# Optimization experiments

Measured on AMD Instinct MI355X. Metric: run time of the kernel, lower is better.

## Reference

```python
import jax, jax.numpy as jnp
from jax import lax
import numpy as np

B, S = 128, 512
TARGET_SIZE = 32
T = TARGET_SIZE + 4  # tag_size, START = T-2, END = T-1


def setup_inputs() -> dict:
    key = jax.random.key(0)
    k1, k2, k3, k4 = jax.random.split(key, 4)
    feats = jax.random.normal(k1, (B, S, T), dtype=jnp.float32)
    # contiguous-prefix mask (lengths in [S//2, S])
    lengths = jax.random.randint(k2, (B,), S // 2, S + 1)
    mask = (jnp.arange(S)[None, :] < lengths[:, None]).astype(jnp.int32)
    tags = jax.random.randint(k3, (B, S), 0, TARGET_SIZE).astype(jnp.int32)
    # learned transitions, with the hard constraints from __init__
    transitions = 0.1 * jax.random.normal(k4, (T, T), dtype=jnp.float32)
    transitions = transitions.at[:, T - 2].set(-1000.0)  # nothing -> START
    transitions = transitions.at[T - 1, :].set(-1000.0)  # END -> nothing
    return {"feats": feats, "transitions": transitions, "mask": mask, "tags": tags}


def _nll(feats, transitions, mask, tags):
    # feats: (B,S,T), transitions: (T,T) with [i,j] = score(prev=i -> cur=j)
    b, s, t = feats.shape
    START, END = t - 2, t - 1
    fdtype = feats.dtype

    feats_t = jnp.swapaxes(feats, 0, 1)   # (S,B,T)
    mask_t = jnp.swapaxes(mask, 0, 1)     # (S,B)

    # ---- forward algorithm (partition function) ----
    # scores[t,b,i,j] = feats[b,t,j] + transitions[i,j]
    part0 = feats_t[0] + transitions[START][None, :]  # (B,T): alpha after step 0

    def step(part, xs):
        f_step, m_step = xs  # (B,T), (B,)
        # cur[b,i,j] = feats[b,j] + trans[i,j] + part[b,i]
        cur = f_step[:, None, :] + transitions[None, :, :] + part[:, :, None]
        new_part = jax.nn.logsumexp(cur, axis=1)  # (B,T)
        part = jnp.where(m_step[:, None].astype(bool), new_part, part)
        return part, None

    part, _ = lax.scan(step, part0, (feats_t[1:], mask_t[1:]))
    final = jax.nn.logsumexp(part[:, :, None] + transitions[None, :, :], axis=1)  # (B,T)
    forward_score = jnp.sum(final[:, END])

    # ---- gold score ----
    tags_i = tags.astype(jnp.int32)
    prev_tags = jnp.concatenate(
        [jnp.full((b, 1), START, dtype=jnp.int32), tags_i[:, :-1]], axis=1)  # (B,S)
    emit = jnp.take_along_axis(feats, tags_i[:, :, None], axis=2)[:, :, 0]    # (B,S)
    trans_sc = transitions[prev_tags, tags_i]                                  # (B,S)
    tg_energy = jnp.sum((emit + trans_sc) * mask.astype(fdtype))
    lengths = jnp.sum(mask, axis=1).astype(jnp.int32)                          # (B,)
    end_ids = jnp.take_along_axis(tags_i, (lengths - 1)[:, None], axis=1)[:, 0]
    end_energy = jnp.sum(transitions[end_ids, END])
    gold_score = tg_energy + end_energy

    # average_batch = True
    return (forward_score - gold_score) / jnp.asarray(b, fdtype)


def reference(feats, transitions, mask, tags):
    return _nll(feats, transitions, mask, tags)
```

## Files before the change

### kernel.cpp

```cpp
#include <hip/hip_runtime.h>


namespace {
constexpr int kB = 128;
constexpr int kS = 512;
constexpr int kT = 36;
constexpr int kStart = 34;
constexpr int kEnd = 35;

__device__ __forceinline__ float readlane_f(float v, int lane) {
    return __builtin_bit_cast(float, __builtin_amdgcn_readlane(__builtin_bit_cast(int, v), lane));
}

__device__ __forceinline__ float wave_sum(float v) {
#pragma unroll
    for (int off = 32; off; off >>= 1) v += __shfl_xor(v, off, 64);
    return v;
}

__device__ __forceinline__ int wave_sum_i(int v) {
#pragma unroll
    for (int off = 32; off; off >>= 1) v += __shfl_xor(v, off, 64);
    return v;
}

#define FOR36(X) \
    X(0, 0) X(1, 1) X(2, 2) X(3, 3) X(4, 0) X(5, 1) X(6, 2) X(7, 3) \
    X(8, 0) X(9, 1) X(10, 2) X(11, 3) X(12, 0) X(13, 1) X(14, 2) X(15, 3) \
    X(16, 0) X(17, 1) X(18, 2) X(19, 3) X(20, 0) X(21, 1) X(22, 2) X(23, 3) \
    X(24, 0) X(25, 1) X(26, 2) X(27, 3) X(28, 0) X(29, 1) X(30, 2) X(31, 3) \
    X(32, 0) X(33, 1) X(34, 2) X(35, 3)

#define FMDECL(n, a) float Fm##n;
#define FMINIT(n, a) Fm##n = __expf(trans[(n)*kT + jc]);
#define BMDECL(n, a) float Bm##n;
#define BMINIT(n, a) Bm##n = __expf(trans[jc * kT + (n)]);
#define FDOT(n, a) v##a = fmaf(readlane_f(q, n), Fm##n, v##a);
#define BDOT(n, a) w##a = fmaf(readlane_f(p, n), Bm##n, w##a);

#define LDF(t) fl[(size_t)(((t) < kS - 1) ? (t) : (kS - 1)) * kT]
#define LDBW(t) fl[(size_t)(((t) > 0) ? (t) : 0) * kT]

__global__ __attribute__((amdgpu_flat_work_group_size(128, 128),
                          amdgpu_waves_per_eu(1, 1)))
void crf_split_kernel(const float* __restrict__ feats,
                      const float* __restrict__ trans,
                      const int* __restrict__ mask,
                      const int* __restrict__ tags,
                      float* __restrict__ out) {
    const int b = blockIdx.x;
    const int tid = threadIdx.x;
    const int w = tid >> 6;
    const int j = tid & 63;
    const int jc = (j < kT) ? j : (kT - 1);
    const float* fbase = feats + (size_t)b * kS * kT;
    const float* fl = fbase + jc;
    const int* mb = mask + b * kS;
    const int* tb = tags + b * kS;

    __shared__ float gbuf[64];
    __shared__ float cbbuf;

    int len = 0;
#pragma unroll
    for (int k = 0; k < kS / 64; ++k) len += mb[k * 64 + j];
    len = wave_sum_i(len);

    float q = 0.f, Cf = 0.f;

    if (w == 1) {
        FOR36(BMDECL)
        FOR36(BMINIT)
        float g = (j < kT) ? __expf(trans[j * kT + kEnd]) : 0.f;
        float Cb = 0.f;

        auto bstep = [&](float eb, int tau) {
            const float p = eb * g;
            float w0 = 0.f, w1 = 0.f, w2 = 0.f, w3 = 0.f;
            FOR36(BDOT)
            const float ng = (w0 + w1) + (w2 + w3);
            g = (tau < len) ? ng : g;
        };
        auto renormB = [&]() {
            const float mg = readlane_f(g, 0);
            g *= __builtin_amdgcn_rcpf(mg);
            Cb += __logf(mg);
        };

        float pA0, pA1, pA2, pA3, pA4, pA5, pA6, pA7;
        float pB0, pB1, pB2, pB3, pB4, pB5, pB6, pB7;
        float eA0, eA1, eA2, eA3, eA4, eA5, eA6, eA7;
        pA0 = LDBW(511); pA1 = LDBW(510); pA2 = LDBW(509); pA3 = LDBW(508);
        pA4 = LDBW(507); pA5 = LDBW(506); pA6 = LDBW(505); pA7 = LDBW(504);
        eA0 = __expf(pA0); eA1 = __expf(pA1); eA2 = __expf(pA2); eA3 = __expf(pA3);
        eA4 = __expf(pA4); eA5 = __expf(pA5); eA6 = __expf(pA6); eA7 = __expf(pA7);

        int it0 = 0;
        while (it0 < kS / 2) {
            pB0 = LDBW(503 - it0); pB1 = LDBW(502 - it0); pB2 = LDBW(501 - it0); pB3 = LDBW(500 - it0);
            pB4 = LDBW(499 - it0); pB5 = LDBW(498 - it0); pB6 = LDBW(497 - it0); pB7 = LDBW(496 - it0);
            bstep(eA0, 511 - it0); bstep(eA1, 510 - it0);
            bstep(eA2, 509 - it0); bstep(eA3, 508 - it0);
            renormB();
            bstep(eA4, 507 - it0); bstep(eA5, 506 - it0);
            bstep(eA6, 505 - it0); bstep(eA7, 504 - it0);
            renormB();
            eA0 = __expf(pB0); eA1 = __expf(pB1); eA2 = __expf(pB2); eA3 = __expf(pB3);
            eA4 = __expf(pB4); eA5 = __expf(pB5); eA6 = __expf(pB6); eA7 = __expf(pB7);

            pA0 = LDBW(495 - it0); pA1 = LDBW(494 - it0); pA2 = LDBW(493 - it0); pA3 = LDBW(492 - it0);
            pA4 = LDBW(491 - it0); pA5 = LDBW(490 - it0); pA6 = LDBW(489 - it0); pA7 = LDBW(488 - it0);
            bstep(eA0, 503 - it0); bstep(eA1, 502 - it0);
            bstep(eA2, 501 - it0); bstep(eA3, 500 - it0);
            renormB();
            bstep(eA4, 499 - it0); bstep(eA5, 498 - it0);
            bstep(eA6, 497 - it0); bstep(eA7, 496 - it0);
            renormB();
            eA0 = __expf(pA0); eA1 = __expf(pA1); eA2 = __expf(pA2); eA3 = __expf(pA3);
            eA4 = __expf(pA4); eA5 = __expf(pA5); eA6 = __expf(pA6); eA7 = __expf(pA7);
            it0 += 16;
        }
        gbuf[j] = g;
        if (j == 0) cbbuf = Cb;
    } else {
        FOR36(FMDECL)
        FOR36(FMINIT)
        const float a0 = (j < kT) ? (fl[0] + trans[kStart * kT + jc]) : -1e30f;
        Cf = readlane_f(a0, 0);
        q = __expf(a0 - Cf);

        auto fstep = [&](float ef, int t) {
            float v0 = 0.f, v1 = 0.f, v2 = 0.f, v3 = 0.f;
            FOR36(FDOT)
            const float nq = ((v0 + v1) + (v2 + v3)) * ef;
            q = (t < kS / 2) ? nq : q;
        };
        auto renormF = [&]() {
            const float mf = readlane_f(q, 0);
            q *= __builtin_amdgcn_rcpf(mf);
            Cf += __logf(mf);
        };

        float pA0, pA1, pA2, pA3, pA4, pA5, pA6, pA7;
        float pB0, pB1, pB2, pB3, pB4, pB5, pB6, pB7;
        float eA0, eA1, eA2, eA3, eA4, eA5, eA6, eA7;
        pA0 = LDF(1); pA1 = LDF(2); pA2 = LDF(3); pA3 = LDF(4);
        pA4 = LDF(5); pA5 = LDF(6); pA6 = LDF(7); pA7 = LDF(8);
        eA0 = __expf(pA0); eA1 = __expf(pA1); eA2 = __expf(pA2); eA3 = __expf(pA3);
        eA4 = __expf(pA4); eA5 = __expf(pA5); eA6 = __expf(pA6); eA7 = __expf(pA7);

        int it0 = 0;
        while (it0 < kS / 2) {
            pB0 = LDF(it0 + 9);  pB1 = LDF(it0 + 10); pB2 = LDF(it0 + 11); pB3 = LDF(it0 + 12);
            pB4 = LDF(it0 + 13); pB5 = LDF(it0 + 14); pB6 = LDF(it0 + 15); pB7 = LDF(it0 + 16);
            fstep(eA0, it0 + 1); fstep(eA1, it0 + 2);
            fstep(eA2, it0 + 3); fstep(eA3, it0 + 4);
            renormF();
            fstep(eA4, it0 + 5); fstep(eA5, it0 + 6);
            fstep(eA6, it0 + 7); fstep(eA7, it0 + 8);
            renormF();
            eA0 = __expf(pB0); eA1 = __expf(pB1); eA2 = __expf(pB2); eA3 = __expf(pB3);
            eA4 = __expf(pB4); eA5 = __expf(pB5); eA6 = __expf(pB6); eA7 = __expf(pB7);

            pA0 = LDF(it0 + 17); pA1 = LDF(it0 + 18); pA2 = LDF(it0 + 19); pA3 = LDF(it0 + 20);
            pA4 = LDF(it0 + 21); pA5 = LDF(it0 + 22); pA6 = LDF(it0 + 23); pA7 = LDF(it0 + 24);
            fstep(eA0, it0 + 9);  fstep(eA1, it0 + 10);
            fstep(eA2, it0 + 11); fstep(eA3, it0 + 12);
            renormF();
            fstep(eA4, it0 + 13); fstep(eA5, it0 + 14);
            fstep(eA6, it0 + 15); fstep(eA7, it0 + 16);
            renormF();
            eA0 = __expf(pA0); eA1 = __expf(pA1); eA2 = __expf(pA2); eA3 = __expf(pA3);
            eA4 = __expf(pA4); eA5 = __expf(pA5); eA6 = __expf(pA6); eA7 = __expf(pA7);
            it0 += 16;
        }
    }

    __syncthreads();

    if (w == 0) {
        const float Z = wave_sum(q * gbuf[j]);
        const float forward_b = Cf + cbbuf + __logf(Z);

        float gold = 0.f;
        for (int k = j; k < kS; k += 64) {
            if (k < len) {
                const int tg = tb[k];
                const int pv = (k == 0) ? kStart : tb[k - 1];
                gold += fbase[(size_t)k * kT + tg] + trans[pv * kT + tg];
            }
        }
        gold = wave_sum(gold);

        if (j == 0) {
            gold += trans[tb[len - 1] * kT + kEnd];
            atomicAdd(out, (forward_b - gold) * (1.0f / kB));
        }
    }
}

}

extern "C" void kernel_launch(void* const* d_in, const int* in_sizes, int n_in,
                              void* d_out, int out_size, void* d_ws, size_t ws_size,
                              hipStream_t stream) {
    const float* feats = (const float*)d_in[0];
    const float* trans = (const float*)d_in[1];
    const int* mask = (const int*)d_in[2];
    const int* tags = (const int*)d_in[3];
    float* out = (float*)d_out;

    (void)hipMemsetAsync(out, 0, sizeof(float), stream);
    crf_split_kernel<<<dim3(kB), dim3(128), 0, stream>>>(feats, trans, mask, tags, out);
}
```

Measured before the change: 102.9 us.

## Trim CRF matvec to 34 source tags and fold renormalization into emissions

Drops the START and END source rows from the per-step dot product, since transitions into START are -1000 and END has no outgoing transitions, so their exp terms are negligible. Moves each renormalization off the recurrence's critical path by scaling the next step's emission factor by the reciprocal instead of rescaling the state. All 34 readlanes are now issued before the FMAs behind a scheduling barrier. The forward loop gets an exact-length tail, which removes the per-step t<S/2 select. This cuts per-step latency on the serial chain, but the 34-row truncation is approximate and relies on the -1000 transition constraints.

```diff
diff --git a/kernel.cpp b/kernel.cpp
--- a/kernel.cpp
+++ b/kernel.cpp
@@ -24,19 +24,20 @@
     return v;
 }
 
-#define FOR36(X) \
+#define FOR34(X) \
     X(0, 0) X(1, 1) X(2, 2) X(3, 3) X(4, 0) X(5, 1) X(6, 2) X(7, 3) \
     X(8, 0) X(9, 1) X(10, 2) X(11, 3) X(12, 0) X(13, 1) X(14, 2) X(15, 3) \
     X(16, 0) X(17, 1) X(18, 2) X(19, 3) X(20, 0) X(21, 1) X(22, 2) X(23, 3) \
     X(24, 0) X(25, 1) X(26, 2) X(27, 3) X(28, 0) X(29, 1) X(30, 2) X(31, 3) \
-    X(32, 0) X(33, 1) X(34, 2) X(35, 3)
+    X(32, 0) X(33, 1)
 
 #define FMDECL(n, a) float Fm##n;
 #define FMINIT(n, a) Fm##n = __expf(trans[(n)*kT + jc]);
 #define BMDECL(n, a) float Bm##n;
 #define BMINIT(n, a) Bm##n = __expf(trans[jc * kT + (n)]);
-#define FDOT(n, a) v##a = fmaf(readlane_f(q, n), Fm##n, v##a);
-#define BDOT(n, a) w##a = fmaf(readlane_f(p, n), Bm##n, w##a);
+#define RLD(n, a) const float s##n = readlane_f(src, n);
+#define FD(n, a) v##a = fmaf(s##n, Fm##n, v##a);
+#define BD(n, a) w##a = fmaf(s##n, Bm##n, w##a);
 
 #define LDF(t) fl[(size_t)(((t) < kS - 1) ? (t) : (kS - 1)) * kT]
 #define LDBW(t) fl[(size_t)(((t) > 0) ? (t) : 0) * kT]
@@ -69,22 +70,25 @@
     float q = 0.f, Cf = 0.f;
 
     if (w == 1) {
-        FOR36(BMDECL)
-        FOR36(BMINIT)
+        FOR34(BMDECL)
+        FOR34(BMINIT)
         float g = (j < kT) ? __expf(trans[j * kT + kEnd]) : 0.f;
         float Cb = 0.f;
 
         auto bstep = [&](float eb, int tau) {
-            const float p = eb * g;
+            const float src = eb * g;
             float w0 = 0.f, w1 = 0.f, w2 = 0.f, w3 = 0.f;
-            FOR36(BDOT)
+            FOR34(RLD)
+            __builtin_amdgcn_sched_barrier(0);
+            FOR34(BD)
             const float ng = (w0 + w1) + (w2 + w3);
             g = (tau < len) ? ng : g;
         };
-        auto renormB = [&]() {
+        auto renormB = [&](float& eb_next, int tau_next) {
             const float mg = readlane_f(g, 0);
-            g *= __builtin_amdgcn_rcpf(mg);
-            Cb += __logf(mg);
+            const float lg = __logf(mg);
+            const float r = __builtin_amdgcn_rcpf(mg);
+            if (tau_next < len) { Cb += lg; eb_next *= r; }
         };
 
         float pA0, pA1, pA2, pA3, pA4, pA5, pA6, pA7;
@@ -101,44 +105,46 @@
             pB4 = LDBW(499 - it0); pB5 = LDBW(498 - it0); pB6 = LDBW(497 - it0); pB7 = LDBW(496 - it0);
             bstep(eA0, 511 - it0); bstep(eA1, 510 - it0);
             bstep(eA2, 509 - it0); bstep(eA3, 508 - it0);
-            renormB();
+            renormB(eA4, 507 - it0);
             bstep(eA4, 507 - it0); bstep(eA5, 506 - it0);
             bstep(eA6, 505 - it0); bstep(eA7, 504 - it0);
-            renormB();
             eA0 = __expf(pB0); eA1 = __expf(pB1); eA2 = __expf(pB2); eA3 = __expf(pB3);
             eA4 = __expf(pB4); eA5 = __expf(pB5); eA6 = __expf(pB6); eA7 = __expf(pB7);
+            renormB(eA0, 503 - it0);
 
             pA0 = LDBW(495 - it0); pA1 = LDBW(494 - it0); pA2 = LDBW(493 - it0); pA3 = LDBW(492 - it0);
             pA4 = LDBW(491 - it0); pA5 = LDBW(490 - it0); pA6 = LDBW(489 - it0); pA7 = LDBW(488 - it0);
             bstep(eA0, 503 - it0); bstep(eA1, 502 - it0);
             bstep(eA2, 501 - it0); bstep(eA3, 500 - it0);
-            renormB();
+            renormB(eA4, 499 - it0);
             bstep(eA4, 499 - it0); bstep(eA5, 498 - it0);
             bstep(eA6, 497 - it0); bstep(eA7, 496 - it0);
-            renormB();
             eA0 = __expf(pA0); eA1 = __expf(pA1); eA2 = __expf(pA2); eA3 = __expf(pA3);
             eA4 = __expf(pA4); eA5 = __expf(pA5); eA6 = __expf(pA6); eA7 = __expf(pA7);
+            if (it0 < kS / 2 - 16) renormB(eA0, 495 - it0);
             it0 += 16;
         }
         gbuf[j] = g;
         if (j == 0) cbbuf = Cb;
     } else {
-        FOR36(FMDECL)
-        FOR36(FMINIT)
+        FOR34(FMDECL)
+        FOR34(FMINIT)
         const float a0 = (j < kT) ? (fl[0] + trans[kStart * kT + jc]) : -1e30f;
         Cf = readlane_f(a0, 0);
         q = __expf(a0 - Cf);
 
-        auto fstep = [&](float ef, int t) {
+        auto fstep = [&](float ef) {
+            const float src = q;
             float v0 = 0.f, v1 = 0.f, v2 = 0.f, v3 = 0.f;
-            FOR36(FDOT)
-            const float nq = ((v0 + v1) + (v2 + v3)) * ef;
-            q = (t < kS / 2) ? nq : q;
-        };
-        auto renormF = [&]() {
+            FOR34(RLD)
+            __builtin_amdgcn_sched_barrier(0);
+            FOR34(FD)
+            q = ((v0 + v1) + (v2 + v3)) * ef;
+        };
+        auto renormF = [&](float& ef_next) {
             const float mf = readlane_f(q, 0);
-            q *= __builtin_amdgcn_rcpf(mf);
             Cf += __logf(mf);
+            ef_next *= __builtin_amdgcn_rcpf(mf);
         };
 
         float pA0, pA1, pA2, pA3, pA4, pA5, pA6, pA7;
@@ -150,30 +156,37 @@
         eA4 = __expf(pA4); eA5 = __expf(pA5); eA6 = __expf(pA6); eA7 = __expf(pA7);
 
         int it0 = 0;
-        while (it0 < kS / 2) {
+        while (it0 < 240) {
             pB0 = LDF(it0 + 9);  pB1 = LDF(it0 + 10); pB2 = LDF(it0 + 11); pB3 = LDF(it0 + 12);
             pB4 = LDF(it0 + 13); pB5 = LDF(it0 + 14); pB6 = LDF(it0 + 15); pB7 = LDF(it0 + 16);
-            fstep(eA0, it0 + 1); fstep(eA1, it0 + 2);
-            fstep(eA2, it0 + 3); fstep(eA3, it0 + 4);
-            renormF();
-            fstep(eA4, it0 + 5); fstep(eA5, it0 + 6);
-            fstep(eA6, it0 + 7); fstep(eA7, it0 + 8);
-            renormF();
+            fstep(eA0); fstep(eA1); fstep(eA2); fstep(eA3);
+            renormF(eA4);
+            fstep(eA4); fstep(eA5); fstep(eA6); fstep(eA7);
             eA0 = __expf(pB0); eA1 = __expf(pB1); eA2 = __expf(pB2); eA3 = __expf(pB3);
             eA4 = __expf(pB4); eA5 = __expf(pB5); eA6 = __expf(pB6); eA7 = __expf(pB7);
+            renormF(eA0);
 
             pA0 = LDF(it0 + 17); pA1 = LDF(it0 + 18); pA2 = LDF(it0 + 19); pA3 = LDF(it0 + 20);
             pA4 = LDF(it0 + 21); pA5 = LDF(it0 + 22); pA6 = LDF(it0 + 23); pA7 = LDF(it0 + 24);
-            fstep(eA0, it0 + 9);  fstep(eA1, it0 + 10);
-            fstep(eA2, it0 + 11); fstep(eA3, it0 + 12);
-            renormF();
-            fstep(eA4, it0 + 13); fstep(eA5, it0 + 14);
-            fstep(eA6, it0 + 15); fstep(eA7, it0 + 16);
-            renormF();
+            fstep(eA0); fstep(eA1); fstep(eA2); fstep(eA3);
+            renormF(eA4);
+            fstep(eA4); fstep(eA5); fstep(eA6); fstep(eA7);
             eA0 = __expf(pA0); eA1 = __expf(pA1); eA2 = __expf(pA2); eA3 = __expf(pA3);
             eA4 = __expf(pA4); eA5 = __expf(pA5); eA6 = __expf(pA6); eA7 = __expf(pA7);
+            renormF(eA0);
             it0 += 16;
         }
+        float pT0 = LDF(249), pT1 = LDF(250), pT2 = LDF(251), pT3 = LDF(252);
+        float pT4 = LDF(253), pT5 = LDF(254), pT6 = LDF(255);
+        fstep(eA0); fstep(eA1); fstep(eA2); fstep(eA3);
+        renormF(eA4);
+        fstep(eA4); fstep(eA5); fstep(eA6); fstep(eA7);
+        float eT0 = __expf(pT0), eT1 = __expf(pT1), eT2 = __expf(pT2), eT3 = __expf(pT3);
+        float eT4 = __expf(pT4), eT5 = __expf(pT5), eT6 = __expf(pT6);
+        renormF(eT0);
+        fstep(eT0); fstep(eT1); fstep(eT2); fstep(eT3);
+        renormF(eT4);
+        fstep(eT4); fstep(eT5); fstep(eT6);
     }
 
     __syncthreads();
```

Result: slower. 106.0 us (+3.0%).

## Replace readlane matvec with DPP ring-rotation matvec across lane groups

Applied to the files above, without the earlier changes.

The per-step 36x36 matrix-vector product is reorganized. Before, it used 36 scalar readlanes per step. Now each lane holds three state components and does a systolic-style ring rotation with DPP row_ror over 16-lane rows, followed by shuffles to gather the result. The aim is to remove the serialized readlane/SALU path and spread the work over lane groups with fewer dependent operations per step. In exchange it adds DPP rotation latency, three ds_bpermute shuffles per step, renormalization once every four steps instead of every four in an eight-step pattern, and more delicate indexing math.

```diff
diff --git a/kernel.cpp b/kernel.cpp
--- a/kernel.cpp
+++ b/kernel.cpp
@@ -11,175 +11,169 @@
 __device__ __forceinline__ float readlane_f(float v, int lane) {
     return __builtin_bit_cast(float, __builtin_amdgcn_readlane(__builtin_bit_cast(int, v), lane));
 }
+__device__ __forceinline__ float ror1_f(float x) {
+    const int xi = __builtin_bit_cast(int, x);
+    return __builtin_bit_cast(float, __builtin_amdgcn_update_dpp(xi, xi, 0x121, 0xF, 0xF, false));
+}
+__device__ __forceinline__ float ror8_f(float x) {
+    const int xi = __builtin_bit_cast(int, x);
+    return __builtin_bit_cast(float, __builtin_amdgcn_update_dpp(xi, xi, 0x128, 0xF, 0xF, false));
+}
 
 __device__ __forceinline__ float wave_sum(float v) {
 #pragma unroll
     for (int off = 32; off; off >>= 1) v += __shfl_xor(v, off, 64);
     return v;
 }
-
 __device__ __forceinline__ int wave_sum_i(int v) {
 #pragma unroll
     for (int off = 32; off; off >>= 1) v += __shfl_xor(v, off, 64);
     return v;
 }
 
-#define FOR36(X) \
-    X(0, 0) X(1, 1) X(2, 2) X(3, 3) X(4, 0) X(5, 1) X(6, 2) X(7, 3) \
-    X(8, 0) X(9, 1) X(10, 2) X(11, 3) X(12, 0) X(13, 1) X(14, 2) X(15, 3) \
-    X(16, 0) X(17, 1) X(18, 2) X(19, 3) X(20, 0) X(21, 1) X(22, 2) X(23, 3) \
-    X(24, 0) X(25, 1) X(26, 2) X(27, 3) X(28, 0) X(29, 1) X(30, 2) X(31, 3) \
-    X(32, 0) X(33, 1) X(34, 2) X(35, 3)
-
-#define FMDECL(n, a) float Fm##n;
-#define FMINIT(n, a) Fm##n = __expf(trans[(n)*kT + jc]);
-#define BMDECL(n, a) float Bm##n;
-#define BMINIT(n, a) Bm##n = __expf(trans[jc * kT + (n)]);
-#define FDOT(n, a) v##a = fmaf(readlane_f(q, n), Fm##n, v##a);
-#define BDOT(n, a) w##a = fmaf(readlane_f(p, n), Bm##n, w##a);
-
-#define LDF(t) fl[(size_t)(((t) < kS - 1) ? (t) : (kS - 1)) * kT]
-#define LDBW(t) fl[(size_t)(((t) > 0) ? (t) : 0) * kT]
+#define FOR8(X) X(0) X(1) X(2) X(3) X(4) X(5) X(6) X(7)
+
+#define XPC(row, col) ((((row) < kT) && ((col) < kT)) ? __expf(trans[(row)*kT + (col)]) : 0.f)
+#define JO(m) (16 * rc + ((p - (m)) & 15))
+
+#define FDU(k) const float DU0_##k = XPC(s0, JO(k)), DU1_##k = XPC(s1, JO(k)), DU2_##k = XPC(s2, JO(k));
+#define FDV(k) const float DV0_##k = XPC(s0, JO(8 + (k))), DV1_##k = XPC(s1, JO(8 + (k))), DV2_##k = XPC(s2, JO(8 + (k)));
+#define BDU(k) const float DU0_##k = XPC(JO(k), s0), DU1_##k = XPC(JO(k), s1), DU2_##k = XPC(JO(k), s2);
+#define BDV(k) const float DV0_##k = XPC(JO(8 + (k)), s0), DV1_##k = XPC(JO(8 + (k)), s1), DV2_##k = XPC(JO(8 + (k)), s2);
+
+#define PHASE(k) \
+    U = fmaf(R0, DU0_##k, U); V = fmaf(R0, DV0_##k, V); \
+    U = fmaf(R1, DU1_##k, U); V = fmaf(R1, DV1_##k, V); \
+    U = fmaf(R2, DU2_##k, U); V = fmaf(R2, DV2_##k, V); \
+    U = ror1_f(U); V = ror1_f(V);
+
+#define LD3(t, s) p##s##x = fl0[(t) * kT]; p##s##y = fl1[(t) * kT]; p##s##z = fl2[(t) * kT];
+#define EX3(s) e##s##x = __expf(p##s##x); e##s##y = __expf(p##s##y); e##s##z = __expf(p##s##z);
 
 __global__ __attribute__((amdgpu_flat_work_group_size(128, 128),
                           amdgpu_waves_per_eu(1, 1)))
-void crf_split_kernel(const float* __restrict__ feats,
-                      const float* __restrict__ trans,
-                      const int* __restrict__ mask,
-                      const int* __restrict__ tags,
-                      float* __restrict__ out) {
+void crf_ring_kernel(const float* __restrict__ feats,
+                     const float* __restrict__ trans,
+                     const int* __restrict__ mask,
+                     const int* __restrict__ tags,
+                     float* __restrict__ out) {
     const int b = blockIdx.x;
     const int tid = threadIdx.x;
     const int w = tid >> 6;
     const int j = tid & 63;
-    const int jc = (j < kT) ? j : (kT - 1);
+    const int p = j & 15;
+    const int rr = j >> 4;
+    const int rc = (rr < 2) ? rr : 2;
+    const int s0 = p, s1 = 16 + p, s2 = 32 + p;
     const float* fbase = feats + (size_t)b * kS * kT;
-    const float* fl = fbase + jc;
+    const float* fl0 = fbase + s0;
+    const float* fl1 = fbase + s1;
+    const float* fl2 = fbase + ((s2 < kT) ? s2 : (kT - 1));
     const int* mb = mask + b * kS;
     const int* tb = tags + b * kS;
 
-    __shared__ float gbuf[64];
+    __shared__ float gbuf[3][64];
     __shared__ float cbbuf;
 
     int len = 0;
 #pragma unroll
     for (int k = 0; k < kS / 64; ++k) len += mb[k * 64 + j];
-    len = wave_sum_i(len);
-
-    float q = 0.f, Cf = 0.f;
+    len = __builtin_amdgcn_readfirstlane(wave_sum_i(len));
+
+    float Q0 = 0.f, Q1 = 0.f, Q2 = 0.f, Cf = 0.f;
+
+    float p0x, p0y, p0z, p1x, p1y, p1z, p2x, p2y, p2z, p3x, p3y, p3z;
+    float e0x, e0y, e0z, e1x, e1y, e1z, e2x, e2y, e2z, e3x, e3y, e3z;
 
     if (w == 1) {
-        FOR36(BMDECL)
-        FOR36(BMINIT)
-        float g = (j < kT) ? __expf(trans[j * kT + kEnd]) : 0.f;
+        FOR8(BDU) FOR8(BDV)
+        float G0 = __expf(trans[s0 * kT + kEnd]);
+        float G1 = __expf(trans[s1 * kT + kEnd]);
+        float G2 = (s2 < kT) ? __expf(trans[s2 * kT + kEnd]) : 0.f;
         float Cb = 0.f;
 
-        auto bstep = [&](float eb, int tau) {
-            const float p = eb * g;
-            float w0 = 0.f, w1 = 0.f, w2 = 0.f, w3 = 0.f;
-            FOR36(BDOT)
-            const float ng = (w0 + w1) + (w2 + w3);
-            g = (tau < len) ? ng : g;
-        };
-        auto renormB = [&]() {
-            const float mg = readlane_f(g, 0);
-            g *= __builtin_amdgcn_rcpf(mg);
-            Cb += __logf(mg);
-        };
-
-        float pA0, pA1, pA2, pA3, pA4, pA5, pA6, pA7;
-        float pB0, pB1, pB2, pB3, pB4, pB5, pB6, pB7;
-        float eA0, eA1, eA2, eA3, eA4, eA5, eA6, eA7;
-        pA0 = LDBW(511); pA1 = LDBW(510); pA2 = LDBW(509); pA3 = LDBW(508);
-        pA4 = LDBW(507); pA5 = LDBW(506); pA6 = LDBW(505); pA7 = LDBW(504);
-        eA0 = __expf(pA0); eA1 = __expf(pA1); eA2 = __expf(pA2); eA3 = __expf(pA3);
-        eA4 = __expf(pA4); eA5 = __expf(pA5); eA6 = __expf(pA6); eA7 = __expf(pA7);
-
-        int it0 = 0;
-        while (it0 < kS / 2) {
-            pB0 = LDBW(503 - it0); pB1 = LDBW(502 - it0); pB2 = LDBW(501 - it0); pB3 = LDBW(500 - it0);
-            pB4 = LDBW(499 - it0); pB5 = LDBW(498 - it0); pB6 = LDBW(497 - it0); pB7 = LDBW(496 - it0);
-            bstep(eA0, 511 - it0); bstep(eA1, 510 - it0);
-            bstep(eA2, 509 - it0); bstep(eA3, 508 - it0);
-            renormB();
-            bstep(eA4, 507 - it0); bstep(eA5, 506 - it0);
-            bstep(eA6, 505 - it0); bstep(eA7, 504 - it0);
-            renormB();
-            eA0 = __expf(pB0); eA1 = __expf(pB1); eA2 = __expf(pB2); eA3 = __expf(pB3);
-            eA4 = __expf(pB4); eA5 = __expf(pB5); eA6 = __expf(pB6); eA7 = __expf(pB7);
-
-            pA0 = LDBW(495 - it0); pA1 = LDBW(494 - it0); pA2 = LDBW(493 - it0); pA3 = LDBW(492 - it0);
-            pA4 = LDBW(491 - it0); pA5 = LDBW(490 - it0); pA6 = LDBW(489 - it0); pA7 = LDBW(488 - it0);
-            bstep(eA0, 503 - it0); bstep(eA1, 502 - it0);
-            bstep(eA2, 501 - it0); bstep(eA3, 500 - it0);
-            renormB();
-            bstep(eA4, 499 - it0); bstep(eA5, 498 - it0);
-            bstep(eA6, 497 - it0); bstep(eA7, 496 - it0);
-            renormB();
-            eA0 = __expf(pA0); eA1 = __expf(pA1); eA2 = __expf(pA2); eA3 = __expf(pA3);
-            eA4 = __expf(pA4); eA5 = __expf(pA5); eA6 = __expf(pA6); eA7 = __expf(pA7);
-            it0 += 16;
-        }
-        gbuf[j] = g;
+        auto bstep = [&](float e0, float e1, float e2, int tau) {
+            const float R0 = e0 * G0, R1 = e1 * G1, R2 = e2 * G2;
+            float U = 0.f, V = 0.f;
+            FOR8(PHASE)
+            const float Y = ror8_f(U) + V;
+            const float n0 = __shfl(Y, s0, 64);
+            const float n1 = __shfl(Y, s1, 64);
+            const float n2 = __shfl(Y, s2, 64);
+            const bool upd = tau < len;
+            G0 = upd ? n0 : G0; G1 = upd ? n1 : G1; G2 = upd ? n2 : G2;
+        };
+        auto renormB = [&](float& e0, float& e1, float& e2, int tau_next) {
+            const float mg = readlane_f(G0, 0);
+            const float lg = __logf(mg);
+            const float rv = __builtin_amdgcn_rcpf(mg);
+            if (tau_next < len) { Cb += lg; e0 *= rv; e1 *= rv; e2 *= rv; }
+        };
+
+        LD3(511, 0) LD3(510, 1) LD3(509, 2) LD3(508, 3)
+        EX3(0) EX3(1) EX3(2) EX3(3)
+        LD3(507, 0) LD3(506, 1) LD3(505, 2) LD3(504, 3)
+
+#pragma unroll 1
+        for (int g = 0; g < 64; ++g) {
+            const int tg = 511 - 4 * g;
+            bstep(e0x, e0y, e0z, tg);
+            bstep(e1x, e1y, e1z, tg - 1);
+            bstep(e2x, e2y, e2z, tg - 2);
+            bstep(e3x, e3y, e3z, tg - 3);
+            EX3(0) EX3(1) EX3(2) EX3(3)
+            LD3(tg - 8, 0) LD3(tg - 9, 1) LD3(tg - 10, 2) LD3(tg - 11, 3)
+            if (g < 63) renormB(e0x, e0y, e0z, tg - 4);
+        }
+        gbuf[0][j] = G0; gbuf[1][j] = G1; gbuf[2][j] = G2;
         if (j == 0) cbbuf = Cb;
     } else {
-        FOR36(FMDECL)
-        FOR36(FMINIT)
-        const float a0 = (j < kT) ? (fl[0] + trans[kStart * kT + jc]) : -1e30f;
-        Cf = readlane_f(a0, 0);
-        q = __expf(a0 - Cf);
-
-        auto fstep = [&](float ef, int t) {
-            float v0 = 0.f, v1 = 0.f, v2 = 0.f, v3 = 0.f;
-            FOR36(FDOT)
-            const float nq = ((v0 + v1) + (v2 + v3)) * ef;
-            q = (t < kS / 2) ? nq : q;
-        };
-        auto renormF = [&]() {
-            const float mf = readlane_f(q, 0);
-            q *= __builtin_amdgcn_rcpf(mf);
+        FOR8(FDU) FOR8(FDV)
+        Cf = fbase[0] + trans[kStart * kT];
+        Q0 = __expf(fl0[0] + trans[kStart * kT + s0] - Cf);
+        Q1 = __expf(fl1[0] + trans[kStart * kT + s1] - Cf);
+        Q2 = (s2 < kT) ? __expf(fl2[0] + trans[kStart * kT + s2] - Cf) : 0.f;
+
+        auto fstep = [&](float e0, float e1, float e2) {
+            const float R0 = Q0, R1 = Q1, R2 = Q2;
+            float U = 0.f, V = 0.f;
+            FOR8(PHASE)
+            const float Y = ror8_f(U) + V;
+            Q0 = __shfl(Y, s0, 64) * e0;
+            Q1 = __shfl(Y, s1, 64) * e1;
+            Q2 = __shfl(Y, s2, 64) * e2;
+        };
+        auto renormF = [&](float& e0, float& e1, float& e2) {
+            const float mf = readlane_f(Q0, 0);
             Cf += __logf(mf);
-        };
-
-        float pA0, pA1, pA2, pA3, pA4, pA5, pA6, pA7;
-        float pB0, pB1, pB2, pB3, pB4, pB5, pB6, pB7;
-        float eA0, eA1, eA2, eA3, eA4, eA5, eA6, eA7;
-        pA0 = LDF(1); pA1 = LDF(2); pA2 = LDF(3); pA3 = LDF(4);
-        pA4 = LDF(5); pA5 = LDF(6); pA6 = LDF(7); pA7 = LDF(8);
-        eA0 = __expf(pA0); eA1 = __expf(pA1); eA2 = __expf(pA2); eA3 = __expf(pA3);
-        eA4 = __expf(pA4); eA5 = __expf(pA5); eA6 = __expf(pA6); eA7 = __expf(pA7);
-
-        int it0 = 0;
-        while (it0 < kS / 2) {
-            pB0 = LDF(it0 + 9);  pB1 = LDF(it0 + 10); pB2 = LDF(it0 + 11); pB3 = LDF(it0 + 12);
-            pB4 = LDF(it0 + 13); pB5 = LDF(it0 + 14); pB6 = LDF(it0 + 15); pB7 = LDF(it0 + 16);
-            fstep(eA0, it0 + 1); fstep(eA1, it0 + 2);
-            fstep(eA2, it0 + 3); fstep(eA3, it0 + 4);
-            renormF();
-            fstep(eA4, it0 + 5); fstep(eA5, it0 + 6);
-            fstep(eA6, it0 + 7); fstep(eA7, it0 + 8);
-            renormF();
-            eA0 = __expf(pB0); eA1 = __expf(pB1); eA2 = __expf(pB2); eA3 = __expf(pB3);
-            eA4 = __expf(pB4); eA5 = __expf(pB5); eA6 = __expf(pB6); eA7 = __expf(pB7);
-
-            pA0 = LDF(it0 + 17); pA1 = LDF(it0 + 18); pA2 = LDF(it0 + 19); pA3 = LDF(it0 + 20);
-            pA4 = LDF(it0 + 21); pA5 = LDF(it0 + 22); pA6 = LDF(it0 + 23); pA7 = LDF(it0 + 24);
-            fstep(eA0, it0 + 9);  fstep(eA1, it0 + 10);
-            fstep(eA2, it0 + 11); fstep(eA3, it0 + 12);
-            renormF();
-            fstep(eA4, it0 + 13); fstep(eA5, it0 + 14);
-            fstep(eA6, it0 + 15); fstep(eA7, it0 + 16);
-            renormF();
-            eA0 = __expf(pA0); eA1 = __expf(pA1); eA2 = __expf(pA2); eA3 = __expf(pA3);
-            eA4 = __expf(pA4); eA5 = __expf(pA5); eA6 = __expf(pA6); eA7 = __expf(pA7);
-            it0 += 16;
-        }
+            const float rv = __builtin_amdgcn_rcpf(mf);
+            e0 *= rv; e1 *= rv; e2 *= rv;
+        };
+
+        LD3(1, 0) LD3(2, 1) LD3(3, 2) LD3(4, 3)
+        EX3(0) EX3(1) EX3(2) EX3(3)
+        LD3(5, 0) LD3(6, 1) LD3(7, 2) LD3(8, 3)
+
+#pragma unroll 1
+        for (int g = 0; g < 63; ++g) {
+            const int t4 = 4 * g + 5;
+            fstep(e0x, e0y, e0z);
+            fstep(e1x, e1y, e1z);
+            fstep(e2x, e2y, e2z);
+            fstep(e3x, e3y, e3z);
+            EX3(0) EX3(1) EX3(2) EX3(3)
+            LD3(t4 + 4, 0) LD3(t4 + 5, 1) LD3(t4 + 6, 2) LD3(t4 + 7, 3)
+            renormF(e0x, e0y, e0z);
+        }
+        fstep(e0x, e0y, e0z);
+        fstep(e1x, e1y, e1z);
+        fstep(e2x, e2y, e2z);
     }
 
     __syncthreads();
 
     if (w == 0) {
-        const float Z = wave_sum(q * gbuf[j]);
+        const float Z = wave_sum(Q0 * gbuf[0][j] + Q1 * gbuf[1][j] + Q2 * gbuf[2][j]) * 0.25f;
         const float forward_b = Cf + cbbuf + __logf(Z);
 
         float gold = 0.f;
@@ -211,5 +205,5 @@
     float* out = (float*)d_out;
 
     (void)hipMemsetAsync(out, 0, sizeof(float), stream);
-    crf_split_kernel<<<dim3(kB), dim3(128), 0, stream>>>(feats, trans, mask, tags, out);
-}
+    crf_ring_kernel<<<dim3(kB), dim3(128), 0, stream>>>(feats, trans, mask, tags, out);
+}
```

Result: slower. 136.8 us (+32.9%).

## Split CRF forward recursion into length-aware segments across eight waves

Applied to the files above, without the earlier changes.

Each sequence is now split into five segments sized from its actual length. Four waves run forward recursions from uniform start vectors and four run backward recursions, and the segments are stitched together with dot products and normalizers to recover the partition function. This shortens the serial critical path per block and skips padded timesteps. It also drops the START/END columns from the inner dot because their transitions are effectively zero after exp. The cost is 512-thread blocks with higher register pressure, a renormalization folded into the emission factor, and some risk to numerical accuracy from the segment-joining algebra.

```diff
diff --git a/kernel.cpp b/kernel.cpp
--- a/kernel.cpp
+++ b/kernel.cpp
@@ -17,40 +17,37 @@
     for (int off = 32; off; off >>= 1) v += __shfl_xor(v, off, 64);
     return v;
 }
-
 __device__ __forceinline__ int wave_sum_i(int v) {
 #pragma unroll
     for (int off = 32; off; off >>= 1) v += __shfl_xor(v, off, 64);
     return v;
 }
 
-#define FOR36(X) \
+#define FOR34(X) \
     X(0, 0) X(1, 1) X(2, 2) X(3, 3) X(4, 0) X(5, 1) X(6, 2) X(7, 3) \
     X(8, 0) X(9, 1) X(10, 2) X(11, 3) X(12, 0) X(13, 1) X(14, 2) X(15, 3) \
     X(16, 0) X(17, 1) X(18, 2) X(19, 3) X(20, 0) X(21, 1) X(22, 2) X(23, 3) \
     X(24, 0) X(25, 1) X(26, 2) X(27, 3) X(28, 0) X(29, 1) X(30, 2) X(31, 3) \
-    X(32, 0) X(33, 1) X(34, 2) X(35, 3)
+    X(32, 0) X(33, 1)
 
 #define FMDECL(n, a) float Fm##n;
 #define FMINIT(n, a) Fm##n = __expf(trans[(n)*kT + jc]);
 #define BMDECL(n, a) float Bm##n;
 #define BMINIT(n, a) Bm##n = __expf(trans[jc * kT + (n)]);
 #define FDOT(n, a) v##a = fmaf(readlane_f(q, n), Fm##n, v##a);
-#define BDOT(n, a) w##a = fmaf(readlane_f(p, n), Bm##n, w##a);
+#define BDOT(n, a) w##a = fmaf(readlane_f(pp, n), Bm##n, w##a);
 
-#define LDF(t) fl[(size_t)(((t) < kS - 1) ? (t) : (kS - 1)) * kT]
-#define LDBW(t) fl[(size_t)(((t) > 0) ? (t) : 0) * kT]
+#define LDT(t) fl[(size_t)(((t) < 0) ? 0 : (((t) > kS - 1) ? (kS - 1) : (t))) * kT]
 
-__global__ __attribute__((amdgpu_flat_work_group_size(128, 128),
-                          amdgpu_waves_per_eu(1, 1)))
-void crf_split_kernel(const float* __restrict__ feats,
-                      const float* __restrict__ trans,
-                      const int* __restrict__ mask,
-                      const int* __restrict__ tags,
-                      float* __restrict__ out) {
+__global__ __attribute__((amdgpu_flat_work_group_size(512, 512)))
+void crf_seg_kernel(const float* __restrict__ feats,
+                    const float* __restrict__ trans,
+                    const int* __restrict__ mask,
+                    const int* __restrict__ tags,
+                    float* __restrict__ out) {
     const int b = blockIdx.x;
     const int tid = threadIdx.x;
-    const int w = tid >> 6;
+    const int wv = tid >> 6;
     const int j = tid & 63;
     const int jc = (j < kT) ? j : (kT - 1);
     const float* fbase = feats + (size_t)b * kS * kT;
@@ -58,129 +55,113 @@
     const int* mb = mask + b * kS;
     const int* tb = tags + b * kS;
 
-    __shared__ float gbuf[64];
-    __shared__ float cbbuf;
+    __shared__ float vec[8][64];
+    __shared__ float cc[8];
 
     int len = 0;
 #pragma unroll
     for (int k = 0; k < kS / 64; ++k) len += mb[k * 64 + j];
-    len = wave_sum_i(len);
+    len = __builtin_amdgcn_readfirstlane(wave_sum_i(len));
 
-    float q = 0.f, Cf = 0.f;
+    const int c = (len + 3) / 5;
+    const int Gp = (c + 3) >> 2;
 
-    if (w == 1) {
-        FOR36(BMDECL)
-        FOR36(BMINIT)
-        float g = (j < kT) ? __expf(trans[j * kT + kEnd]) : 0.f;
-        float Cb = 0.f;
+    float C = 0.f;
 
-        auto bstep = [&](float eb, int tau) {
-            const float p = eb * g;
-            float w0 = 0.f, w1 = 0.f, w2 = 0.f, w3 = 0.f;
-            FOR36(BDOT)
-            const float ng = (w0 + w1) + (w2 + w3);
-            g = (tau < len) ? ng : g;
-        };
-        auto renormB = [&]() {
-            const float mg = readlane_f(g, 0);
-            g *= __builtin_amdgcn_rcpf(mg);
-            Cb += __logf(mg);
+    if (wv < 4) {
+        FOR34(FMDECL)
+        FOR34(FMINIT)
+        const int t0 = 1 + wv * c;
+        const int cnt = c;
+        float q;
+        if (wv == 0) {
+            const float a0 = (j < kT) ? (fl[0] + trans[kStart * kT + jc]) : -1e30f;
+            C = readlane_f(a0, 0);
+            q = __expf(a0 - C);
+        } else {
+            q = (jc == kStart) ? 0.f : 1.f;
+        }
+
+        auto fstep = [&](float ef, int s) {
+            float v0 = 0.f, v1 = 0.f, v2 = 0.f, v3 = 0.f;
+            FOR34(FDOT)
+            const float nq = ((v0 + v1) + (v2 + v3)) * ef;
+            q = (s < cnt) ? nq : q;
         };
 
-        float pA0, pA1, pA2, pA3, pA4, pA5, pA6, pA7;
-        float pB0, pB1, pB2, pB3, pB4, pB5, pB6, pB7;
-        float eA0, eA1, eA2, eA3, eA4, eA5, eA6, eA7;
-        pA0 = LDBW(511); pA1 = LDBW(510); pA2 = LDBW(509); pA3 = LDBW(508);
-        pA4 = LDBW(507); pA5 = LDBW(506); pA6 = LDBW(505); pA7 = LDBW(504);
-        eA0 = __expf(pA0); eA1 = __expf(pA1); eA2 = __expf(pA2); eA3 = __expf(pA3);
-        eA4 = __expf(pA4); eA5 = __expf(pA5); eA6 = __expf(pA6); eA7 = __expf(pA7);
+        float p0, p1, p2, p3, e0, e1, e2, e3;
+        p0 = LDT(t0 + 0); p1 = LDT(t0 + 1); p2 = LDT(t0 + 2); p3 = LDT(t0 + 3);
+        e0 = __expf(p0); e1 = __expf(p1); e2 = __expf(p2); e3 = __expf(p3);
+        p0 = LDT(t0 + 4); p1 = LDT(t0 + 5); p2 = LDT(t0 + 6); p3 = LDT(t0 + 7);
 
-        int it0 = 0;
-        while (it0 < kS / 2) {
-            pB0 = LDBW(503 - it0); pB1 = LDBW(502 - it0); pB2 = LDBW(501 - it0); pB3 = LDBW(500 - it0);
-            pB4 = LDBW(499 - it0); pB5 = LDBW(498 - it0); pB6 = LDBW(497 - it0); pB7 = LDBW(496 - it0);
-            bstep(eA0, 511 - it0); bstep(eA1, 510 - it0);
-            bstep(eA2, 509 - it0); bstep(eA3, 508 - it0);
-            renormB();
-            bstep(eA4, 507 - it0); bstep(eA5, 506 - it0);
-            bstep(eA6, 505 - it0); bstep(eA7, 504 - it0);
-            renormB();
-            eA0 = __expf(pB0); eA1 = __expf(pB1); eA2 = __expf(pB2); eA3 = __expf(pB3);
-            eA4 = __expf(pB4); eA5 = __expf(pB5); eA6 = __expf(pB6); eA7 = __expf(pB7);
+#pragma unroll 1
+        for (int g = 0; g < Gp; ++g) {
+            const int s = 4 * g;
+            fstep(e0, s); fstep(e1, s + 1); fstep(e2, s + 2); fstep(e3, s + 3);
+            e0 = __expf(p0); e1 = __expf(p1); e2 = __expf(p2); e3 = __expf(p3);
+            p0 = LDT(t0 + s + 8);  p1 = LDT(t0 + s + 9);
+            p2 = LDT(t0 + s + 10); p3 = LDT(t0 + s + 11);
+            if (s + 4 < cnt) {
+                const float mf = readlane_f(q, 0);
+                C += __logf(mf);
+                e0 *= __builtin_amdgcn_rcpf(mf);
+            }
+        }
+        vec[wv][j] = q;
+        if (j == 0) cc[wv] = C;
+    } else {
+        FOR34(BMDECL)
+        FOR34(BMINIT)
+        const bool real = (wv == 7);
+        const int tau0 = real ? (len - 1) : ((wv - 2) * c);
+        const int cnt = real ? (len - 1 - 4 * c) : c;
+        float gg = real ? __expf(trans[jc * kT + kEnd])
+                        : ((jc == kEnd) ? 0.f : 1.f);
 
-            pA0 = LDBW(495 - it0); pA1 = LDBW(494 - it0); pA2 = LDBW(493 - it0); pA3 = LDBW(492 - it0);
-            pA4 = LDBW(491 - it0); pA5 = LDBW(490 - it0); pA6 = LDBW(489 - it0); pA7 = LDBW(488 - it0);
-            bstep(eA0, 503 - it0); bstep(eA1, 502 - it0);
-            bstep(eA2, 501 - it0); bstep(eA3, 500 - it0);
-            renormB();
-            bstep(eA4, 499 - it0); bstep(eA5, 498 - it0);
-            bstep(eA6, 497 - it0); bstep(eA7, 496 - it0);
-            renormB();
-            eA0 = __expf(pA0); eA1 = __expf(pA1); eA2 = __expf(pA2); eA3 = __expf(pA3);
-            eA4 = __expf(pA4); eA5 = __expf(pA5); eA6 = __expf(pA6); eA7 = __expf(pA7);
-            it0 += 16;
-        }
-        gbuf[j] = g;
-        if (j == 0) cbbuf = Cb;
-    } else {
-        FOR36(FMDECL)
-        FOR36(FMINIT)
-        const float a0 = (j < kT) ? (fl[0] + trans[kStart * kT + jc]) : -1e30f;
-        Cf = readlane_f(a0, 0);
-        q = __expf(a0 - Cf);
-
-        auto fstep = [&](float ef, int t) {
-            float v0 = 0.f, v1 = 0.f, v2 = 0.f, v3 = 0.f;
-            FOR36(FDOT)
-            const float nq = ((v0 + v1) + (v2 + v3)) * ef;
-            q = (t < kS / 2) ? nq : q;
-        };
-        auto renormF = [&]() {
-            const float mf = readlane_f(q, 0);
-            q *= __builtin_amdgcn_rcpf(mf);
-            Cf += __logf(mf);
+        auto bstep = [&](float eb, int s) {
+            const float pp = eb * gg;
+            float w0 = 0.f, w1 = 0.f, w2 = 0.f, w3 = 0.f;
+            FOR34(BDOT)
+            const float ng = (w0 + w1) + (w2 + w3);
+            gg = (s < cnt) ? ng : gg;
         };
 
-        float pA0, pA1, pA2, pA3, pA4, pA5, pA6, pA7;
-        float pB0, pB1, pB2, pB3, pB4, pB5, pB6, pB7;
-        float eA0, eA1, eA2, eA3, eA4, eA5, eA6, eA7;
-        pA0 = LDF(1); pA1 = LDF(2); pA2 = LDF(3); pA3 = LDF(4);
-        pA4 = LDF(5); pA5 = LDF(6); pA6 = LDF(7); pA7 = LDF(8);
-        eA0 = __expf(pA0); eA1 = __expf(pA1); eA2 = __expf(pA2); eA3 = __expf(pA3);
-        eA4 = __expf(pA4); eA5 = __expf(pA5); eA6 = __expf(pA6); eA7 = __expf(pA7);
+        float p0, p1, p2, p3, e0, e1, e2, e3;
+        p0 = LDT(tau0 - 0); p1 = LDT(tau0 - 1); p2 = LDT(tau0 - 2); p3 = LDT(tau0 - 3);
+        e0 = __expf(p0); e1 = __expf(p1); e2 = __expf(p2); e3 = __expf(p3);
+        p0 = LDT(tau0 - 4); p1 = LDT(tau0 - 5); p2 = LDT(tau0 - 6); p3 = LDT(tau0 - 7);
 
-        int it0 = 0;
-        while (it0 < kS / 2) {
-            pB0 = LDF(it0 + 9);  pB1 = LDF(it0 + 10); pB2 = LDF(it0 + 11); pB3 = LDF(it0 + 12);
-            pB4 = LDF(it0 + 13); pB5 = LDF(it0 + 14); pB6 = LDF(it0 + 15); pB7 = LDF(it0 + 16);
-            fstep(eA0, it0 + 1); fstep(eA1, it0 + 2);
-            fstep(eA2, it0 + 3); fstep(eA3, it0 + 4);
-            renormF();
-            fstep(eA4, it0 + 5); fstep(eA5, it0 + 6);
-            fstep(eA6, it0 + 7); fstep(eA7, it0 + 8);
-            renormF();
-            eA0 = __expf(pB0); eA1 = __expf(pB1); eA2 = __expf(pB2); eA3 = __expf(pB3);
-            eA4 = __expf(pB4); eA5 = __expf(pB5); eA6 = __expf(pB6); eA7 = __expf(pB7);
-
-            pA0 = LDF(it0 + 17); pA1 = LDF(it0 + 18); pA2 = LDF(it0 + 19); pA3 = LDF(it0 + 20);
-            pA4 = LDF(it0 + 21); pA5 = LDF(it0 + 22); pA6 = LDF(it0 + 23); pA7 = LDF(it0 + 24);
-            fstep(eA0, it0 + 9);  fstep(eA1, it0 + 10);
-            fstep(eA2, it0 + 11); fstep(eA3, it0 + 12);
-            renormF();
-            fstep(eA4, it0 + 13); fstep(eA5, it0 + 14);
-            fstep(eA6, it0 + 15); fstep(eA7, it0 + 16);
-            renormF();
-            eA0 = __expf(pA0); eA1 = __expf(pA1); eA2 = __expf(pA2); eA3 = __expf(pA3);
-            eA4 = __expf(pA4); eA5 = __expf(pA5); eA6 = __expf(pA6); eA7 = __expf(pA7);
-            it0 += 16;
+#pragma unroll 1
+        for (int g = 0; g < Gp; ++g) {
+            const int s = 4 * g;
+            bstep(e0, s); bstep(e1, s + 1); bstep(e2, s + 2); bstep(e3, s + 3);
+            e0 = __expf(p0); e1 = __expf(p1); e2 = __expf(p2); e3 = __expf(p3);
+            p0 = LDT(tau0 - s - 8);  p1 = LDT(tau0 - s - 9);
+            p2 = LDT(tau0 - s - 10); p3 = LDT(tau0 - s - 11);
+            if (s + 4 < cnt) {
+                const float mg = readlane_f(gg, 0);
+                C += __logf(mg);
+                e0 *= __builtin_amdgcn_rcpf(mg);
+            }
         }
+        vec[wv][j] = gg;
+        if (j == 0) cc[wv] = C;
     }
 
     __syncthreads();
 
-    if (w == 0) {
-        const float Z = wave_sum(q * gbuf[j]);
-        const float forward_b = Cf + cbbuf + __logf(Z);
+    if (wv == 0) {
+        const float msk = (j < kT) ? 1.f : 0.f;
+        const float d1 = wave_sum(msk * vec[4][j] * vec[0][j]);
+        const float d2 = wave_sum(msk * vec[5][j] * vec[1][j]);
+        const float d3 = wave_sum(msk * vec[6][j] * vec[2][j]);
+        const float d4 = wave_sum(msk * vec[7][j] * vec[3][j]);
+        const float n1 = wave_sum(msk * vec[1][j]);
+        const float n2 = wave_sum(msk * vec[2][j]);
+        const float n3 = wave_sum(msk * vec[3][j]);
+        const float forward_b = cc[0] + cc[4] + cc[5] + cc[6] + cc[7]
+            + __logf(d1) + __logf(d2) + __logf(d3) + __logf(d4)
+            - __logf(n1) - __logf(n2) - __logf(n3);
 
         float gold = 0.f;
         for (int k = j; k < kS; k += 64) {
@@ -211,5 +192,5 @@
     float* out = (float*)d_out;
 
     (void)hipMemsetAsync(out, 0, sizeof(float), stream);
-    crf_split_kernel<<<dim3(kB), dim3(128), 0, stream>>>(feats, trans, mask, tags, out);
+    crf_seg_kernel<<<dim3(kB), dim3(512), 0, stream>>>(feats, trans, mask, tags, out);
 }
```

New measurement: 98.95 us. -3.8%, faster.
